# Kernel tuning notes

Measured on AMD Instinct MI355X. Metric: run time of the kernel, lower is better.

## Reference

```python
import jax, jax.numpy as jnp
import numpy as np

B, C, H, W = 16, 512, 64, 64


def setup_inputs() -> dict:
    key = jax.random.key(0)
    k1, k2 = jax.random.split(key)
    img_feat = jax.random.normal(k1, (B, C, H, W), dtype=jnp.float32)
    text_feat = jax.random.normal(k2, (B, C, H, W), dtype=jnp.float32)
    gamma = jnp.zeros((1,), dtype=jnp.float32)
    return {"img_feat": img_feat, "text_feat": text_feat, "gamma": gamma}


def reference(img_feat, text_feat, gamma):
    b, c, h, w = img_feat.shape
    q = img_feat.reshape(b, c, h * w)          # [B, C, HW]
    kv = text_feat.reshape(b, c, h * w)        # [B, C, HW]
    # channel-attention map: [B, C, C]
    attn = jnp.einsum('bcn,bdn->bcd', q, kv)
    attn = jax.nn.softmax(attn, axis=-1)
    info = jnp.einsum('bcd,bdn->bcn', attn, kv).reshape(b, c, h, w)
    return gamma * info + img_feat
```

## Files before the change

kernel.cpp:

```cpp
#include <hip/hip_runtime.h>
#include <hip/hip_bf16.h>


constexpr int NB = 16;
constexpr int NC = 512;
constexpr int NHW = 4096;

typedef float f32x4 __attribute__((ext_vector_type(4)));
typedef __bf16 bf16x4 __attribute__((ext_vector_type(4)));
typedef __bf16 bf16x8 __attribute__((ext_vector_type(8)));

__device__ __forceinline__ void gload16(const void* g, void* l) {
  __builtin_amdgcn_global_load_lds(
      (const __attribute__((address_space(1))) void*)g,
      (__attribute__((address_space(3))) void*)l, 16, 0, 0);
}

template <int EPI, int MDIM, int NDIM, int KDIM, int SPLITS>
__global__ __launch_bounds__(512, 4) void gemm_bt(
    const __bf16* __restrict__ A, const __bf16* __restrict__ B,
    float* __restrict__ Dp, const float* __restrict__ img,
    const float* __restrict__ gammap, float* __restrict__ outp) {
  __shared__ __bf16 sA[2][128 * 64];
  __shared__ __bf16 sB[2][128 * 64];

  const int t = threadIdx.x;
  const int lane = t & 63;
  const int wave = t >> 6;
  const int wr = wave >> 2;
  const int wc = wave & 3;

  constexpr int GX = MDIM / 128;
  constexpr int GY = NDIM / 128;
  constexpr int NWG = GX * GY * NB * SPLITS;
  constexpr int QX = NWG / 8;
  int flat = blockIdx.x + GX * (blockIdx.y + GY * blockIdx.z);
  flat = (flat & 7) * QX + (flat >> 3);
  const int bx = flat % GX;
  const int by = (flat / GX) % GY;
  const int bz = flat / (GX * GY);
  const int batch = bz / SPLITS;
  const int split = bz % SPLITS;

  const int aRow0 = bx * 128;
  const int bRow0 = by * 128;
  constexpr int KSUB = KDIM / SPLITS;
  constexpr int NT = KSUB / 64;
  const int kBeg = split * KSUB;

  const int rl = lane >> 3;
  const int csrc = ((lane & 7) ^ rl) * 8;
  const __bf16* Abase = A + (long)batch * MDIM * KDIM +
                        (long)(aRow0 + wave * 16 + rl) * KDIM + csrc + kBeg;
  const __bf16* Bbase = B + (long)batch * NDIM * KDIM +
                        (long)(bRow0 + wave * 16 + rl) * KDIM + csrc + kBeg;
  const int ldsOff = wave * 16 * 64;

  auto stage = [&](int buf, int kof) {
#pragma unroll
    for (int i = 0; i < 2; ++i) {
      gload16(Abase + kof + (long)i * 8 * KDIM, &sA[buf][ldsOff + i * 8 * 64]);
      gload16(Bbase + kof + (long)i * 8 * KDIM, &sB[buf][ldsOff + i * 8 * 64]);
    }
  };

  f32x4 acc[4][2] = {};

  auto compute_tile = [&](int buf) {
#pragma unroll
    for (int kk = 0; kk < 2; ++kk) {
      const int kb = kk * 32 + ((lane >> 4) << 3);
      bf16x8 af[4], bfr[2];
#pragma unroll
      for (int m = 0; m < 4; ++m) {
        const int r = wr * 64 + m * 16 + (lane & 15);
        af[m] = *(const bf16x8*)&sA[buf][r * 64 + (kb ^ ((r & 7) << 3))];
      }
#pragma unroll
      for (int n = 0; n < 2; ++n) {
        const int r = wc * 32 + n * 16 + (lane & 15);
        bfr[n] = *(const bf16x8*)&sB[buf][r * 64 + (kb ^ ((r & 7) << 3))];
      }
#pragma unroll
      for (int m = 0; m < 4; ++m)
#pragma unroll
        for (int n = 0; n < 2; ++n)
          acc[m][n] = __builtin_amdgcn_mfma_f32_16x16x32_bf16(
              af[m], bfr[n], acc[m][n], 0, 0, 0);
    }
  };

  stage(0, 0);
  int cur = 0;
#pragma unroll 1
  for (int tt = 0; tt < NT - 1; ++tt) {
    stage(cur ^ 1, (tt + 1) * 64);
    asm volatile("s_waitcnt vmcnt(4)" ::: "memory");
    __builtin_amdgcn_s_barrier();
    compute_tile(cur);
    __builtin_amdgcn_s_barrier();
    cur ^= 1;
  }
  asm volatile("s_waitcnt vmcnt(0)" ::: "memory");
  __builtin_amdgcn_s_barrier();
  compute_tile(cur);

  if constexpr (EPI == 0) {
    float* D = Dp + ((long)split * NB + batch) * MDIM * NDIM;
    const int m0 = aRow0 + wr * 64;
    const int n0 = bRow0 + wc * 32;
#pragma unroll
    for (int m = 0; m < 4; ++m)
#pragma unroll
      for (int n = 0; n < 2; ++n) {
        const int row0 = m0 + m * 16 + ((lane >> 4) << 2);
        const int col = n0 + n * 16 + (lane & 15);
#pragma unroll
        for (int r = 0; r < 4; ++r)
          D[(long)(row0 + r) * NDIM + col] = acc[m][n][r];
      }
  } else {
    const float g = gammap[0];
    const long obase = (long)batch * NC * NHW;
    const int sp0 = aRow0 + wr * 64;
    const int ch0 = bRow0 + wc * 32;
#pragma unroll
    for (int m = 0; m < 4; ++m)
#pragma unroll
      for (int n = 0; n < 2; ++n) {
        const int sp = sp0 + m * 16 + ((lane >> 4) << 2);
        const int ch = ch0 + n * 16 + (lane & 15);
        const long idx = obase + (long)ch * NHW + sp;
        f32x4 iv = *(const f32x4*)(img + idx);
        f32x4 ov;
#pragma unroll
        for (int r = 0; r < 4; ++r) ov[r] = g * acc[m][n][r] + iv[r];
        *(f32x4*)(outp + idx) = ov;
      }
  }
}

__global__ __launch_bounds__(256) void cast_q(const float* __restrict__ src,
                                              __bf16* __restrict__ dst) {
  const long N = (long)NB * NC * NHW;
  const long stride = (long)gridDim.x * 256 * 8;
  for (long i = ((long)blockIdx.x * 256 + threadIdx.x) * 8; i < N; i += stride) {
    f32x4 a = *(const f32x4*)(src + i);
    f32x4 b = *(const f32x4*)(src + i + 4);
    bf16x8 h = {(__bf16)a.x, (__bf16)a.y, (__bf16)a.z, (__bf16)a.w,
                (__bf16)b.x, (__bf16)b.y, (__bf16)b.z, (__bf16)b.w};
    *(bf16x8*)(dst + i) = h;
  }
}

__global__ __launch_bounds__(256) void prep_kv(const float* __restrict__ kv,
                                               __bf16* __restrict__ kv16,
                                               __bf16* __restrict__ kvT) {
  __shared__ __bf16 tile[64 * 68];
  const int t = threadIdx.x;
  const int n0 = blockIdx.x * 64;
  const int d0 = blockIdx.y * 64;
  const long ibase = (long)blockIdx.z * NC * NHW;

  const int nc4 = (t & 15) * 4;
  const int dr0 = t >> 4;
#pragma unroll
  for (int i = 0; i < 4; ++i) {
    const int dr = dr0 + 16 * i;
    f32x4 v = *(const f32x4*)(kv + ibase + (long)(d0 + dr) * NHW + n0 + nc4);
    bf16x4 h = {(__bf16)v.x, (__bf16)v.y, (__bf16)v.z, (__bf16)v.w};
    *(bf16x4*)&tile[dr * 68 + nc4] = h;
    *(bf16x4*)(kv16 + ibase + (long)(d0 + dr) * NHW + n0 + nc4) = h;
  }
  __syncthreads();

  const long obase = (long)blockIdx.z * NHW * NC;
  const int nr = t >> 2;
  const int dc0 = t & 3;
#pragma unroll
  for (int i = 0; i < 2; ++i) {
    const int dc = dc0 + 4 * i;
    bf16x8 pk;
#pragma unroll
    for (int j = 0; j < 8; ++j) pk[j] = tile[(dc * 8 + j) * 68 + nr];
    *(bf16x8*)(kvT + obase + (long)(n0 + nr) * NC + d0 + dc * 8) = pk;
  }
}

template <int SPLITS>
__global__ __launch_bounds__(256) void softmax_rows(
    const float* __restrict__ attn, __bf16* __restrict__ P) {
  const int row = blockIdx.x * 4 + (threadIdx.x >> 6);
  const int lane = threadIdx.x & 63;
  const long PS = (long)NB * NC * NC;
  const float* src = attn + (long)row * NC;

  float x[8] = {0.f, 0.f, 0.f, 0.f, 0.f, 0.f, 0.f, 0.f};
#pragma unroll
  for (int s = 0; s < SPLITS; ++s) {
    f32x4 v0 = *(const f32x4*)(src + s * PS + lane * 4);
    f32x4 v1 = *(const f32x4*)(src + s * PS + 256 + lane * 4);
#pragma unroll
    for (int r = 0; r < 4; ++r) { x[r] += v0[r]; x[4 + r] += v1[r]; }
  }

  float mx = x[0];
#pragma unroll
  for (int r = 1; r < 8; ++r) mx = fmaxf(mx, x[r]);
#pragma unroll
  for (int off = 32; off >= 1; off >>= 1) mx = fmaxf(mx, __shfl_xor(mx, off));

  float e[8], s = 0.f;
#pragma unroll
  for (int r = 0; r < 8; ++r) { e[r] = expf(x[r] - mx); s += e[r]; }
#pragma unroll
  for (int off = 32; off >= 1; off >>= 1) s += __shfl_xor(s, off);
  const float inv = 1.0f / s;

  __bf16* dst = P + (long)row * NC;
  bf16x4 h0, h1;
#pragma unroll
  for (int r = 0; r < 4; ++r) {
    h0[r] = (__bf16)(e[r] * inv);
    h1[r] = (__bf16)(e[4 + r] * inv);
  }
  *(bf16x4*)(dst + lane * 4) = h0;
  *(bf16x4*)(dst + 256 + lane * 4) = h1;
}

extern "C" void kernel_launch(void* const* d_in, const int* in_sizes, int n_in,
                              void* d_out, int out_size, void* d_ws,
                              size_t ws_size, hipStream_t stream) {
  const float* img = (const float*)d_in[0];
  const float* txt = (const float*)d_in[1];
  const float* gamma = (const float*)d_in[2];
  float* out = (float*)d_out;

  __bf16* q16 = (__bf16*)d_out;
  __bf16* kv16 = (__bf16*)d_out + (size_t)NB * NC * NHW;

  const size_t MiB = 1024 * 1024;
  char* ws = (char*)d_ws;
  const bool big = ws_size >= 104 * MiB;

  float* attnP = (float*)ws;
  __bf16* P = (__bf16*)(ws + (big ? 32 : 16) * MiB);
  __bf16* kvT = (__bf16*)(ws + (big ? 40 : 24) * MiB);

  cast_q<<<2048, 256, 0, stream>>>(img, q16);
  prep_kv<<<dim3(NHW / 64, NC / 64, NB), 256, 0, stream>>>(txt, kv16, kvT);

  if (big)
    gemm_bt<0, NC, NC, NHW, 2><<<dim3(4, 4, NB * 2), 512, 0, stream>>>(
        q16, kv16, attnP, nullptr, nullptr, nullptr);
  else
    gemm_bt<0, NC, NC, NHW, 1><<<dim3(4, 4, NB), 512, 0, stream>>>(
        q16, kv16, attnP, nullptr, nullptr, nullptr);

  if (big)
    softmax_rows<2><<<dim3(NB * NC / 4), 256, 0, stream>>>(attnP, P);
  else
    softmax_rows<1><<<dim3(NB * NC / 4), 256, 0, stream>>>(attnP, P);

  gemm_bt<1, NHW, NC, NC, 1><<<dim3(NHW / 128, 4, NB), 512, 0, stream>>>(
      kvT, P, nullptr, img, gamma, out);
}
```

Measured before the change: 242.7 us.

## Fuse fp32-to-bf16 cast of Q into QK GEMM and simplify PV GEMM

Drops the separate cast_q kernel and instead has the QK GEMM load img directly as fp32 into registers, convert to bf16 and write it into swizzled LDS while B is staged asynchronously. This avoids writing and re-reading a bf16 copy of Q in global memory. The PV GEMM becomes a dedicated kernel with single-buffered LDS and plain __syncthreads, losing the double-buffer overlap. Workspace layout is also reassigned so that kvT and P live in d_ws and the attention partials sit in d_out.

Result: faster. 216.1 us (-10.9%).

```diff
diff --git a/kernel.cpp b/kernel.cpp
--- a/kernel.cpp
+++ b/kernel.cpp
@@ -5,6 +5,7 @@
 constexpr int NB = 16;
 constexpr int NC = 512;
 constexpr int NHW = 4096;
+constexpr int QKSPLIT = 2;
 
 typedef float f32x4 __attribute__((ext_vector_type(4)));
 typedef __bf16 bf16x4 __attribute__((ext_vector_type(4)));
@@ -16,11 +17,10 @@
       (__attribute__((address_space(3))) void*)l, 16, 0, 0);
 }
 
-template <int EPI, int MDIM, int NDIM, int KDIM, int SPLITS>
-__global__ __launch_bounds__(512, 4) void gemm_bt(
-    const __bf16* __restrict__ A, const __bf16* __restrict__ B,
-    float* __restrict__ Dp, const float* __restrict__ img,
-    const float* __restrict__ gammap, float* __restrict__ outp) {
+template <int SPLITS>
+__global__ __launch_bounds__(512) void gemm_qk(const float* __restrict__ Af,
+                                               const __bf16* __restrict__ B,
+                                               float* __restrict__ Dp) {
   __shared__ __bf16 sA[2][128 * 64];
   __shared__ __bf16 sB[2][128 * 64];
 
@@ -30,42 +30,57 @@
   const int wr = wave >> 2;
   const int wc = wave & 3;
 
-  constexpr int GX = MDIM / 128;
-  constexpr int GY = NDIM / 128;
-  constexpr int NWG = GX * GY * NB * SPLITS;
+  constexpr int NWG = 16 * NB * SPLITS;
   constexpr int QX = NWG / 8;
-  int flat = blockIdx.x + GX * (blockIdx.y + GY * blockIdx.z);
+  int flat = blockIdx.x + 4 * (blockIdx.y + 4 * blockIdx.z);
   flat = (flat & 7) * QX + (flat >> 3);
-  const int bx = flat % GX;
-  const int by = (flat / GX) % GY;
-  const int bz = flat / (GX * GY);
+  const int bx = flat & 3;
+  const int by = (flat >> 2) & 3;
+  const int bz = flat >> 4;
   const int batch = bz / SPLITS;
   const int split = bz % SPLITS;
 
   const int aRow0 = bx * 128;
   const int bRow0 = by * 128;
-  constexpr int KSUB = KDIM / SPLITS;
+  constexpr int KSUB = NHW / SPLITS;
   constexpr int NT = KSUB / 64;
   const int kBeg = split * KSUB;
 
   const int rl = lane >> 3;
   const int csrc = ((lane & 7) ^ rl) * 8;
-  const __bf16* Abase = A + (long)batch * MDIM * KDIM +
-                        (long)(aRow0 + wave * 16 + rl) * KDIM + csrc + kBeg;
-  const __bf16* Bbase = B + (long)batch * NDIM * KDIM +
-                        (long)(bRow0 + wave * 16 + rl) * KDIM + csrc + kBeg;
+  const __bf16* Bbase = B + (long)batch * NC * NHW +
+                        (long)(bRow0 + wave * 16 + rl) * NHW + csrc + kBeg;
   const int ldsOff = wave * 16 * 64;
 
-  auto stage = [&](int buf, int kof) {
-#pragma unroll
-    for (int i = 0; i < 2; ++i) {
-      gload16(Abase + kof + (long)i * 8 * KDIM, &sA[buf][ldsOff + i * 8 * 64]);
-      gload16(Bbase + kof + (long)i * 8 * KDIM, &sB[buf][ldsOff + i * 8 * 64]);
-    }
+  const int c4 = (t & 15) * 4;
+  const int rb = t >> 4;
+  const float* Abase =
+      Af + (long)batch * NC * NHW + (long)(aRow0 + rb) * NHW + kBeg + c4;
+
+  f32x4 ra[4];
+  auto loadA = [&](int kof) {
+#pragma unroll
+    for (int i = 0; i < 4; ++i)
+      ra[i] = *(const f32x4*)(Abase + kof + (long)(32 * i) * NHW);
   };
+  auto writeA = [&](int buf) {
+#pragma unroll
+    for (int i = 0; i < 4; ++i) {
+      const int r = rb + 32 * i;
+      const int idx = r * 64 + (c4 ^ ((r & 7) << 3));
+      bf16x4 h = {(__bf16)ra[i].x, (__bf16)ra[i].y, (__bf16)ra[i].z,
+                  (__bf16)ra[i].w};
+      *(bf16x4*)&sA[buf][idx] = h;
+    }
+  };
+  auto stageB = [&](int buf, int kof) {
+#pragma unroll
+    for (int i = 0; i < 2; ++i)
+      gload16(Bbase + kof + (long)(i * 8) * NHW,
+              &sB[buf][ldsOff + i * 8 * 64]);
+  };
 
   f32x4 acc[4][2] = {};
-
   auto compute_tile = [&](int buf) {
 #pragma unroll
     for (int kk = 0; kk < 2; ++kk) {
@@ -90,67 +105,132 @@
     }
   };
 
-  stage(0, 0);
+  stageB(0, 0);
+  loadA(0);
+  asm volatile("s_waitcnt vmcnt(0)" ::: "memory");
+  writeA(0);
+  __syncthreads();
+
   int cur = 0;
 #pragma unroll 1
-  for (int tt = 0; tt < NT - 1; ++tt) {
-    stage(cur ^ 1, (tt + 1) * 64);
-    asm volatile("s_waitcnt vmcnt(4)" ::: "memory");
-    __builtin_amdgcn_s_barrier();
+  for (int tt = 0; tt < NT; ++tt) {
+    const bool more = (tt + 1) < NT;
+    if (more) {
+      stageB(cur ^ 1, (tt + 1) * 64);
+      loadA((tt + 1) * 64);
+      asm volatile("" ::: "memory");
+    }
     compute_tile(cur);
-    __builtin_amdgcn_s_barrier();
-    cur ^= 1;
-  }
-  asm volatile("s_waitcnt vmcnt(0)" ::: "memory");
-  __builtin_amdgcn_s_barrier();
-  compute_tile(cur);
-
-  if constexpr (EPI == 0) {
-    float* D = Dp + ((long)split * NB + batch) * MDIM * NDIM;
-    const int m0 = aRow0 + wr * 64;
-    const int n0 = bRow0 + wc * 32;
-#pragma unroll
-    for (int m = 0; m < 4; ++m)
+    if (more) {
+      __builtin_amdgcn_s_barrier();
+      asm volatile("s_waitcnt vmcnt(0)" ::: "memory");
+      writeA(cur ^ 1);
+      asm volatile("s_waitcnt lgkmcnt(0)" ::: "memory");
+      __builtin_amdgcn_s_barrier();
+      cur ^= 1;
+    }
+  }
+
+  float* D = Dp + ((long)split * NB + batch) * NC * NC;
+  const int m0 = aRow0 + wr * 64;
+  const int n0 = bRow0 + wc * 32;
+#pragma unroll
+  for (int m = 0; m < 4; ++m)
+#pragma unroll
+    for (int n = 0; n < 2; ++n) {
+      const int row0 = m0 + m * 16 + ((lane >> 4) << 2);
+      const int col = n0 + n * 16 + (lane & 15);
+#pragma unroll
+      for (int r = 0; r < 4; ++r)
+        D[(long)(row0 + r) * NC + col] = acc[m][n][r];
+    }
+}
+
+__global__ __launch_bounds__(512) void gemm_pv(const __bf16* __restrict__ A,
+                                               const __bf16* __restrict__ B,
+                                               const float* __restrict__ img,
+                                               const float* __restrict__ gammap,
+                                               float* __restrict__ outp) {
+  __shared__ __bf16 sA[128 * 64];
+  __shared__ __bf16 sB[128 * 64];
+
+  const int t = threadIdx.x;
+  const int lane = t & 63;
+  const int wave = t >> 6;
+  const int wr = wave >> 2;
+  const int wc = wave & 3;
+
+  constexpr int GX = NHW / 128;
+  constexpr int NWG = GX * 4 * NB;
+  constexpr int QX = NWG / 8;
+  int flat = blockIdx.x + GX * (blockIdx.y + 4 * blockIdx.z);
+  flat = (flat & 7) * QX + (flat >> 3);
+  const int bx = flat % GX;
+  const int by = (flat / GX) & 3;
+  const int batch = flat / (GX * 4);
+
+  const int aRow0 = bx * 128;
+  const int bRow0 = by * 128;
+
+  const int rl = lane >> 3;
+  const int csrc = ((lane & 7) ^ rl) * 8;
+  const __bf16* Abase =
+      A + (long)batch * NHW * NC + (long)(aRow0 + wave * 16 + rl) * NC + csrc;
+  const __bf16* Bbase =
+      B + (long)batch * NC * NC + (long)(bRow0 + wave * 16 + rl) * NC + csrc;
+  const int ldsOff = wave * 16 * 64;
+
+  f32x4 acc[4][2] = {};
+
+#pragma unroll 1
+  for (int k0 = 0; k0 < NC; k0 += 64) {
+#pragma unroll
+    for (int i = 0; i < 2; ++i) {
+      gload16(Abase + k0 + (long)(i * 8) * NC, &sA[ldsOff + i * 8 * 64]);
+      gload16(Bbase + k0 + (long)(i * 8) * NC, &sB[ldsOff + i * 8 * 64]);
+    }
+    __syncthreads();
+#pragma unroll
+    for (int kk = 0; kk < 2; ++kk) {
+      const int kb = kk * 32 + ((lane >> 4) << 3);
+      bf16x8 af[4], bfr[2];
+#pragma unroll
+      for (int m = 0; m < 4; ++m) {
+        const int r = wr * 64 + m * 16 + (lane & 15);
+        af[m] = *(const bf16x8*)&sA[r * 64 + (kb ^ ((r & 7) << 3))];
+      }
 #pragma unroll
       for (int n = 0; n < 2; ++n) {
-        const int row0 = m0 + m * 16 + ((lane >> 4) << 2);
-        const int col = n0 + n * 16 + (lane & 15);
-#pragma unroll
-        for (int r = 0; r < 4; ++r)
-          D[(long)(row0 + r) * NDIM + col] = acc[m][n][r];
+        const int r = wc * 32 + n * 16 + (lane & 15);
+        bfr[n] = *(const bf16x8*)&sB[r * 64 + (kb ^ ((r & 7) << 3))];
       }
-  } else {
-    const float g = gammap[0];
-    const long obase = (long)batch * NC * NHW;
-    const int sp0 = aRow0 + wr * 64;
-    const int ch0 = bRow0 + wc * 32;
-#pragma unroll
-    for (int m = 0; m < 4; ++m)
-#pragma unroll
-      for (int n = 0; n < 2; ++n) {
-        const int sp = sp0 + m * 16 + ((lane >> 4) << 2);
-        const int ch = ch0 + n * 16 + (lane & 15);
-        const long idx = obase + (long)ch * NHW + sp;
-        f32x4 iv = *(const f32x4*)(img + idx);
-        f32x4 ov;
-#pragma unroll
-        for (int r = 0; r < 4; ++r) ov[r] = g * acc[m][n][r] + iv[r];
-        *(f32x4*)(outp + idx) = ov;
-      }
-  }
-}
-
-__global__ __launch_bounds__(256) void cast_q(const float* __restrict__ src,
-                                              __bf16* __restrict__ dst) {
-  const long N = (long)NB * NC * NHW;
-  const long stride = (long)gridDim.x * 256 * 8;
-  for (long i = ((long)blockIdx.x * 256 + threadIdx.x) * 8; i < N; i += stride) {
-    f32x4 a = *(const f32x4*)(src + i);
-    f32x4 b = *(const f32x4*)(src + i + 4);
-    bf16x8 h = {(__bf16)a.x, (__bf16)a.y, (__bf16)a.z, (__bf16)a.w,
-                (__bf16)b.x, (__bf16)b.y, (__bf16)b.z, (__bf16)b.w};
-    *(bf16x8*)(dst + i) = h;
-  }
+#pragma unroll
+      for (int m = 0; m < 4; ++m)
+#pragma unroll
+        for (int n = 0; n < 2; ++n)
+          acc[m][n] = __builtin_amdgcn_mfma_f32_16x16x32_bf16(
+              af[m], bfr[n], acc[m][n], 0, 0, 0);
+    }
+    __syncthreads();
+  }
+
+  const float g = gammap[0];
+  const long obase = (long)batch * NC * NHW;
+  const int sp0 = aRow0 + wr * 64;
+  const int ch0 = bRow0 + wc * 32;
+#pragma unroll
+  for (int m = 0; m < 4; ++m)
+#pragma unroll
+    for (int n = 0; n < 2; ++n) {
+      const int sp = sp0 + m * 16 + ((lane >> 4) << 2);
+      const int ch = ch0 + n * 16 + (lane & 15);
+      const long idx = obase + (long)ch * NHW + sp;
+      f32x4 iv = *(const f32x4*)(img + idx);
+      f32x4 ov;
+#pragma unroll
+      for (int r = 0; r < 4; ++r) ov[r] = g * acc[m][n][r] + iv[r];
+      *(f32x4*)(outp + idx) = ov;
+    }
 }
 
 __global__ __launch_bounds__(256) void prep_kv(const float* __restrict__ kv,
@@ -236,32 +316,18 @@
   const float* gamma = (const float*)d_in[2];
   float* out = (float*)d_out;
 
-  __bf16* q16 = (__bf16*)d_out;
-  __bf16* kv16 = (__bf16*)d_out + (size_t)NB * NC * NHW;
-
   const size_t MiB = 1024 * 1024;
-  char* ws = (char*)d_ws;
-  const bool big = ws_size >= 104 * MiB;
-
-  float* attnP = (float*)ws;
-  __bf16* P = (__bf16*)(ws + (big ? 32 : 16) * MiB);
-  __bf16* kvT = (__bf16*)(ws + (big ? 40 : 24) * MiB);
-
-  cast_q<<<2048, 256, 0, stream>>>(img, q16);
+  __bf16* kv16 = (__bf16*)d_out;
+  float* attnP = (float*)((char*)d_out + 68 * MiB);
+  __bf16* kvT = (__bf16*)d_ws;
+  __bf16* P = (__bf16*)((char*)d_ws + 64 * MiB);
+
   prep_kv<<<dim3(NHW / 64, NC / 64, NB), 256, 0, stream>>>(txt, kv16, kvT);
 
-  if (big)
-    gemm_bt<0, NC, NC, NHW, 2><<<dim3(4, 4, NB * 2), 512, 0, stream>>>(
-        q16, kv16, attnP, nullptr, nullptr, nullptr);
-  else
-    gemm_bt<0, NC, NC, NHW, 1><<<dim3(4, 4, NB), 512, 0, stream>>>(
-        q16, kv16, attnP, nullptr, nullptr, nullptr);
-
-  if (big)
-    softmax_rows<2><<<dim3(NB * NC / 4), 256, 0, stream>>>(attnP, P);
-  else
-    softmax_rows<1><<<dim3(NB * NC / 4), 256, 0, stream>>>(attnP, P);
-
-  gemm_bt<1, NHW, NC, NC, 1><<<dim3(NHW / 128, 4, NB), 512, 0, stream>>>(
-      kvT, P, nullptr, img, gamma, out);
-}
+  gemm_qk<QKSPLIT><<<dim3(4, 4, NB * QKSPLIT), 512, 0, stream>>>(
+      img, kv16, attnP);
+
+  softmax_rows<QKSPLIT><<<dim3(NB * NC / 4), 256, 0, stream>>>(attnP, P);
+
+  gemm_pv<<<dim3(NHW / 128, 4, NB), 512, 0, stream>>>(kvT, P, img, gamma, out);
+}
```
